# Performance work log

Measured on AMD Instinct MI355X. Metric: run time of the kernel, lower is better.

## Reference

```python
import jax, jax.numpy as jnp
import numpy as np

N = 512          # N_ROIs (nodes)
E = N * N        # number of edges
V = 6            # number of views (edge_attr dim)
DIMS = [(1, 36), (36, 24), (24, 5)]  # (in, out) per NNConv layer


def _nnconv(x, edge_attr, src, dst, We, be, root, bias, cin, cout):
    # edge MLP: Linear + ReLU -> per-edge weight matrix [E, cin, cout]
    w = jax.nn.relu(edge_attr @ We + be).reshape(-1, cin, cout)
    msg = jnp.einsum('ei,eio->eo', x[src], w)              # gather + per-edge matmul
    s = jax.ops.segment_sum(msg, dst, num_segments=N)      # scatter-sum
    cnt = jax.ops.segment_sum(jnp.ones((msg.shape[0], 1), x.dtype), dst, num_segments=N)
    agg = s / jnp.maximum(cnt, 1.0)                        # mean aggregation
    return agg + x @ root + bias                           # root weight + bias (PyG NNConv)


def setup_inputs() -> dict:
    key = jax.random.key(0)
    ks = jax.random.split(key, 16)
    x = jnp.ones((N, 1), jnp.float32)
    edge_attr = jax.random.uniform(ks[0], (E, V), jnp.float32)
    edge_index = jax.random.randint(ks[1], (2, E), 0, N, dtype=jnp.int32)
    inp = {'x': x, 'edge_attr': edge_attr, 'edge_index': edge_index}
    for l, (cin, cout) in enumerate(DIMS, start=1):
        k = jax.random.split(ks[1 + l], 4)
        inp[f'We{l}'] = jax.random.normal(k[0], (V, cin * cout), jnp.float32) / np.sqrt(V)
        inp[f'be{l}'] = jnp.zeros((cin * cout,), jnp.float32)
        inp[f'root{l}'] = jax.random.normal(k[1], (cin, cout), jnp.float32) / np.sqrt(cin)
        inp[f'b{l}'] = jnp.zeros((cout,), jnp.float32)
    return inp


def reference(x, edge_attr, edge_index,
              We1, be1, root1, b1,
              We2, be2, root2, b2,
              We3, be3, root3, b3):
    src, dst = edge_index[0], edge_index[1]
    h = jax.nn.relu(_nnconv(x, edge_attr, src, dst, We1, be1, root1, b1, *DIMS[0]))
    h = jax.nn.relu(_nnconv(h, edge_attr, src, dst, We2, be2, root2, b2, *DIMS[1]))
    h = jax.nn.relu(_nnconv(h, edge_attr, src, dst, We3, be3, root3, b3, *DIMS[2]))
    # pairwise CBT: sum_k |h_i,k - h_j,k|  ->  [N, N]
    cbt = jnp.sum(jnp.abs(h[:, None, :] - h[None, :, :]), axis=2)
    return cbt
```

## Files before the change

### kernel.cpp

```cpp
#include <hip/hip_runtime.h>
#include <hip/hip_bf16.h>

#define N_NODES 512
#define N_EDGES (512 * 512)
#define NBLK 256
#define EPB (N_EDGES / NBLK)

typedef __attribute__((ext_vector_type(2))) _Float16 half2v;

#if defined(__has_builtin)
#if __has_builtin(__builtin_amdgcn_fdot2)
#define FDOT2(a, b, c) __builtin_amdgcn_fdot2((a), (b), (c), false)
#endif
#endif
#ifndef FDOT2
static __device__ inline float fdot2_sw(half2v a, half2v b, float c) {
    return (float)a.x * (float)b.x + (float)a.y * (float)b.y + c;
}
#define FDOT2(a, b, c) fdot2_sw((a), (b), (c))
#endif

static __device__ inline unsigned pack_h2(float x, float y) {
    union { _Float16 h[2]; unsigned u; } c;
    c.h[0] = (_Float16)x;
    c.h[1] = (_Float16)y;
    return c.u;
}
static __device__ inline half2v bits_h2(int b) {
    union { int i; half2v h; } c;
    c.i = b;
    return c.h;
}

__global__ __launch_bounds__(256) void count_kernel(const int* __restrict__ dst,
                                                    int* __restrict__ bcnt) {
    __shared__ int h[N_NODES];
    int tid = threadIdx.x;
    int b = blockIdx.x;
    h[tid] = 0;
    h[tid + 256] = 0;
    __syncthreads();
#pragma unroll
    for (int k = 0; k < EPB / 256; k++)
        atomicAdd(&h[dst[b * EPB + k * 256 + tid]], 1);
    __syncthreads();
    bcnt[b * N_NODES + tid] = h[tid];
    bcnt[b * N_NODES + tid + 256] = h[tid + 256];
}

__global__ __launch_bounds__(512) void scan_kernel(const int* __restrict__ bcnt,
                                                   int* __restrict__ offs,
                                                   int* __restrict__ base) {
    __shared__ int buf[N_NODES];
    int t = threadIdx.x;
    int sum = 0;
    for (int b = 0; b < NBLK; b++) sum += bcnt[b * N_NODES + t];
    buf[t] = sum;
    __syncthreads();
    for (int d = 1; d < N_NODES; d <<= 1) {
        int add = (t >= d) ? buf[t - d] : 0;
        __syncthreads();
        buf[t] += add;
        __syncthreads();
    }
    offs[t + 1] = buf[t];
    if (t == 0) offs[0] = 0;
    int run = buf[t] - sum;
    for (int b = 0; b < NBLK; b++) {
        base[b * N_NODES + t] = run;
        run += bcnt[b * N_NODES + t];
    }
}

__global__ __launch_bounds__(256) void scatter_kernel(const int* __restrict__ src,
                                                      const int* __restrict__ dst,
                                                      const float* __restrict__ ea,
                                                      const int* __restrict__ base,
                                                      int4* __restrict__ ed4) {
    __shared__ int lcur[N_NODES];
    int tid = threadIdx.x;
    int b = blockIdx.x;
    lcur[tid] = base[b * N_NODES + tid];
    lcur[tid + 256] = base[b * N_NODES + tid + 256];
    __syncthreads();
#pragma unroll
    for (int k = 0; k < EPB / 256; k++) {
        int e = b * EPB + k * 256 + tid;
        const float* a = ea + (size_t)e * 6;
        float a0 = a[0], a1 = a[1], a2 = a[2], a3 = a[3], a4 = a[4], a5 = a[5];
        int p = atomicAdd(&lcur[dst[e]], 1);
        int4 r;
        r.x = (int)pack_h2(a0, a1);
        r.y = (int)pack_h2(a2, a3);
        r.z = (int)pack_h2(a4, a5);
        r.w = src[e];
        ed4[p] = r;
    }
}

template <int CIN, int COUT, int OG, int BLK, int G>
__global__ __launch_bounds__(BLK) void nnconv_edges(
    const float* __restrict__ hprev,
    const int4* __restrict__ ed4,
    const int* __restrict__ offs,
    const float* __restrict__ We,
    const float* __restrict__ be,
    float* __restrict__ agg)
{
    constexpr int J = CIN * COUT;
    constexpr int OPL = COUT / OG;
    constexpr int A = CIN * OPL;

    const int n = blockIdx.x / G;
    const int g = blockIdx.x % G;
    const int tid = threadIdx.x;
    const bool act = (tid < A);
    const int i = act ? tid / OPL : 0;
    const int og = act ? (tid % OPL) * OG : 0;

    half2v wrp[OG][3];
    float ber[OG], acc[OG];
#pragma unroll
    for (int k = 0; k < OG; k++) {
        acc[k] = 0.f;
        int j = i * COUT + og + k;
        if (act) {
            ber[k] = be[j];
#pragma unroll
            for (int t = 0; t < 3; t++)
                wrp[k][t] = bits_h2((int)pack_h2(We[(2 * t) * J + j], We[(2 * t + 1) * J + j]));
        } else {
            ber[k] = 0.f;
#pragma unroll
            for (int t = 0; t < 3; t++) wrp[k][t] = bits_h2(0);
        }
    }

    const int start = offs[n];
    const int end = offs[n + 1];
    const int len = end - start;
    const int per = (len + G - 1) / G;
    int p = start + g * per;
    int p1 = p + per;
    if (p1 > end) p1 = end;

    const float* hp_i = hprev + i;

    for (; p + 8 <= p1; p += 8) {
        const int4* eb = ed4 + p;
        int4 ed[8];
#pragma unroll
        for (int u = 0; u < 8; u++) ed[u] = eb[u];
        float xv[8];
#pragma unroll
        for (int u = 0; u < 8; u++) xv[u] = hp_i[ed[u].w * CIN];
#pragma unroll
        for (int u = 0; u < 8; u++) {
            half2v e01 = bits_h2(ed[u].x), e23 = bits_h2(ed[u].y), e45 = bits_h2(ed[u].z);
#pragma unroll
            for (int k = 0; k < OG; k++) {
                float z = FDOT2(e45, wrp[k][2],
                        FDOT2(e23, wrp[k][1],
                        FDOT2(e01, wrp[k][0], ber[k])));
                acc[k] = fmaf(xv[u], fmaxf(z, 0.f), acc[k]);
            }
        }
    }
    for (; p < p1; ++p) {
        int4 ed = ed4[p];
        float xv = hp_i[ed.w * CIN];
        half2v e01 = bits_h2(ed.x), e23 = bits_h2(ed.y), e45 = bits_h2(ed.z);
#pragma unroll
        for (int k = 0; k < OG; k++) {
            float z = FDOT2(e45, wrp[k][2],
                    FDOT2(e23, wrp[k][1],
                    FDOT2(e01, wrp[k][0], ber[k])));
            acc[k] = fmaf(xv, fmaxf(z, 0.f), acc[k]);
        }
    }

    if constexpr (CIN == 1) {
        if (act) atomicAdd(&agg[n * COUT + og], acc[0]);
    } else {
        __shared__ float lds_acc[J];
        if (act) {
#pragma unroll
            for (int k = 0; k < OG; k++) lds_acc[i * COUT + og + k] = acc[k];
        }
        __syncthreads();
        if (tid < COUT) {
            float sum = 0.f;
#pragma unroll
            for (int ii = 0; ii < CIN; ii++) sum += lds_acc[ii * COUT + tid];
            atomicAdd(&agg[n * COUT + tid], sum);
        }
    }
}

template <int CIN, int COUT>
__global__ __launch_bounds__(64) void nnconv_fin(const float* __restrict__ agg,
                                                 const int* __restrict__ offs,
                                                 const float* __restrict__ hprev,
                                                 const float* __restrict__ root,
                                                 const float* __restrict__ bias,
                                                 float* __restrict__ hout) {
    int n = blockIdx.x;
    int t = threadIdx.x;
    if (t >= COUT) return;
    int cnt = offs[n + 1] - offs[n];
    float inv = 1.f / fmaxf((float)cnt, 1.f);
    float v = agg[n * COUT + t] * inv;
#pragma unroll
    for (int i = 0; i < CIN; i++) v = fmaf(hprev[n * CIN + i], root[i * COUT + t], v);
    v += bias[t];
    hout[n * COUT + t] = fmaxf(v, 0.f);
}

__global__ __launch_bounds__(256) void cbt_kernel(const float* __restrict__ h3,
                                                  float* __restrict__ out) {
    __shared__ float lh[N_NODES * 5];
    int tid = threadIdx.x;
    for (int idx = tid; idx < N_NODES * 5; idx += 256) lh[idx] = h3[idx];
    __syncthreads();
    int i = blockIdx.x;
    float hi[5];
#pragma unroll
    for (int k = 0; k < 5; k++) hi[k] = lh[i * 5 + k];
    for (int j = tid; j < N_NODES; j += 256) {
        float sacc = 0.f;
#pragma unroll
        for (int k = 0; k < 5; k++) sacc += fabsf(hi[k] - lh[j * 5 + k]);
        out[i * N_NODES + j] = sacc;
    }
}

extern "C" void kernel_launch(void* const* d_in, const int* in_sizes, int n_in,
                              void* d_out, int out_size, void* d_ws, size_t ws_size,
                              hipStream_t stream) {
    const float* x = (const float*)d_in[0];
    const float* edge_attr = (const float*)d_in[1];
    const int* edge_index = (const int*)d_in[2];
    const float* We1 = (const float*)d_in[3];
    const float* be1 = (const float*)d_in[4];
    const float* root1 = (const float*)d_in[5];
    const float* b1 = (const float*)d_in[6];
    const float* We2 = (const float*)d_in[7];
    const float* be2 = (const float*)d_in[8];
    const float* root2 = (const float*)d_in[9];
    const float* b2 = (const float*)d_in[10];
    const float* We3 = (const float*)d_in[11];
    const float* be3 = (const float*)d_in[12];
    const float* root3 = (const float*)d_in[13];
    const float* b3 = (const float*)d_in[14];

    const int E = N_EDGES;
    const int* src = edge_index;
    const int* dst = edge_index + E;

    char* ws = (char*)d_ws;
    int* offs = (int*)(ws + 0);
    int* bcnt = (int*)(ws + 4096);
    int* base = (int*)(ws + 528384);
    int4* ed4 = (int4*)(ws + 1052672);
    float* agg1 = (float*)(ws + 5246976);
    float* agg2 = (float*)(ws + 5320704);
    float* agg3 = (float*)(ws + 5369856);
    float* h1 = (float*)(ws + 5380096);
    float* h2 = (float*)(ws + 5453824);
    float* h3 = (float*)(ws + 5502976);

    hipMemsetAsync(agg1, 0, 5380096 - 5246976, stream);

    count_kernel<<<NBLK, 256, 0, stream>>>(dst, bcnt);
    scan_kernel<<<1, 512, 0, stream>>>(bcnt, offs, base);
    scatter_kernel<<<NBLK, 256, 0, stream>>>(src, dst, edge_attr, base, ed4);

    nnconv_edges<1, 36, 1, 64, 16><<<N_NODES * 16, 64, 0, stream>>>(x, ed4, offs, We1, be1, agg1);
    nnconv_fin<1, 36><<<N_NODES, 64, 0, stream>>>(agg1, offs, x, root1, b1, h1);

    nnconv_edges<36, 24, 4, 256, 8><<<N_NODES * 8, 256, 0, stream>>>(h1, ed4, offs, We2, be2, agg2);
    nnconv_fin<36, 24><<<N_NODES, 64, 0, stream>>>(agg2, offs, h1, root2, b2, h2);

    nnconv_edges<24, 5, 1, 128, 8><<<N_NODES * 8, 128, 0, stream>>>(h2, ed4, offs, We3, be3, agg3);
    nnconv_fin<24, 5><<<N_NODES, 64, 0, stream>>>(agg3, offs, h2, root3, b3, h3);

    cbt_kernel<<<N_NODES, 256, 0, stream>>>(h3, (float*)d_out);
}
```

Measured before the change: 202.5 us.

## Compute NNConv edge MLP with bf16 MFMA over padded per-node edge tiles

```diff
diff --git a/kernel.cpp b/kernel.cpp
--- a/kernel.cpp
+++ b/kernel.cpp
@@ -1,35 +1,27 @@
 #include <hip/hip_runtime.h>
 #include <hip/hip_bf16.h>
+#include <hip/hip_fp16.h>
 
 #define N_NODES 512
 #define N_EDGES (512 * 512)
 #define NBLK 256
 #define EPB (N_EDGES / NBLK)
-
-typedef __attribute__((ext_vector_type(2))) _Float16 half2v;
-
-#if defined(__has_builtin)
-#if __has_builtin(__builtin_amdgcn_fdot2)
-#define FDOT2(a, b, c) __builtin_amdgcn_fdot2((a), (b), (c), false)
-#endif
-#endif
-#ifndef FDOT2
-static __device__ inline float fdot2_sw(half2v a, half2v b, float c) {
-    return (float)a.x * (float)b.x + (float)a.y * (float)b.y + c;
-}
-#define FDOT2(a, b, c) fdot2_sw((a), (b), (c))
-#endif
-
-static __device__ inline unsigned pack_h2(float x, float y) {
-    union { _Float16 h[2]; unsigned u; } c;
-    c.h[0] = (_Float16)x;
-    c.h[1] = (_Float16)y;
-    return c.u;
-}
-static __device__ inline half2v bits_h2(int b) {
-    union { int i; half2v h; } c;
-    c.i = b;
-    return c.h;
+#define PADLEN 768
+
+typedef __attribute__((ext_vector_type(8))) __bf16 bf16x8;
+typedef __attribute__((ext_vector_type(16))) float f32x16;
+
+static __device__ inline unsigned bf16rne(float f) {
+    union { float f; unsigned u; } c;
+    c.f = f;
+    unsigned u = c.u;
+    u += 0x7FFFu + ((u >> 16) & 1u);
+    return u >> 16;
+}
+static __device__ inline float bf2f(unsigned h) {
+    union { unsigned u; float f; } c;
+    c.u = h << 16;
+    return c.f;
 }
 
 __global__ __launch_bounds__(256) void count_kernel(const int* __restrict__ dst,
@@ -54,6 +46,7 @@
     __shared__ int buf[N_NODES];
     int t = threadIdx.x;
     int sum = 0;
+#pragma unroll 16
     for (int b = 0; b < NBLK; b++) sum += bcnt[b * N_NODES + t];
     buf[t] = sum;
     __syncthreads();
@@ -66,6 +59,7 @@
     offs[t + 1] = buf[t];
     if (t == 0) offs[0] = 0;
     int run = buf[t] - sum;
+#pragma unroll 16
     for (int b = 0; b < NBLK; b++) {
         base[b * N_NODES + t] = run;
         run += bcnt[b * N_NODES + t];
@@ -76,144 +70,171 @@
                                                       const int* __restrict__ dst,
                                                       const float* __restrict__ ea,
                                                       const int* __restrict__ base,
-                                                      int4* __restrict__ ed4) {
+                                                      const int* __restrict__ offs,
+                                                      int4* __restrict__ edp,
+                                                      int* __restrict__ srcp) {
     __shared__ int lcur[N_NODES];
+    __shared__ int loff[N_NODES];
     int tid = threadIdx.x;
     int b = blockIdx.x;
     lcur[tid] = base[b * N_NODES + tid];
     lcur[tid + 256] = base[b * N_NODES + tid + 256];
-    __syncthreads();
+    loff[tid] = offs[tid];
+    loff[tid + 256] = offs[tid + 256];
+    __syncthreads();
+    const unsigned ONE = 0x3F80u;
 #pragma unroll
     for (int k = 0; k < EPB / 256; k++) {
         int e = b * EPB + k * 256 + tid;
         const float* a = ea + (size_t)e * 6;
-        float a0 = a[0], a1 = a[1], a2 = a[2], a3 = a[3], a4 = a[4], a5 = a[5];
-        int p = atomicAdd(&lcur[dst[e]], 1);
-        int4 r;
-        r.x = (int)pack_h2(a0, a1);
-        r.y = (int)pack_h2(a2, a3);
-        r.z = (int)pack_h2(a4, a5);
-        r.w = src[e];
-        ed4[p] = r;
-    }
-}
-
-template <int CIN, int COUT, int OG, int BLK, int G>
-__global__ __launch_bounds__(BLK) void nnconv_edges(
+        unsigned e0 = bf16rne(a[0]), e1 = bf16rne(a[1]), e2 = bf16rne(a[2]);
+        unsigned e3 = bf16rne(a[3]), e4 = bf16rne(a[4]), e5 = bf16rne(a[5]);
+        int dv = dst[e], sv = src[e];
+        int p = atomicAdd(&lcur[dv], 1);
+        int rank = p - loff[dv];
+        size_t pi = (size_t)dv * PADLEN + rank;
+        int4 r0, r1;
+        r0.x = (int)((e1 << 16) | e0);
+        r0.y = (int)((e3 << 16) | e2);
+        r0.z = (int)((e5 << 16) | e4);
+        r0.w = (int)((e0 << 16) | ONE);
+        r1.x = (int)((e2 << 16) | e1);
+        r1.y = (int)((e4 << 16) | e3);
+        r1.z = (int)((ONE << 16) | e5);
+        r1.w = 0;
+        edp[pi * 2] = r0;
+        edp[pi * 2 + 1] = r1;
+        srcp[pi] = sv;
+    }
+}
+
+__global__ __launch_bounds__(256) void wprep_kernel(const float* __restrict__ We,
+                                                    const float* __restrict__ be,
+                                                    int Jr, int total,
+                                                    int4* __restrict__ wtg) {
+    int idx = blockIdx.x * 256 + threadIdx.x;
+    if (idx >= total) return;
+    int t = idx >> 6, lane = idx & 63, col = lane & 31, hi = lane >> 5;
+    int j = t * 32 + col;
+    unsigned h[8] = {0, 0, 0, 0, 0, 0, 0, 0};
+    if (j < Jr) {
+        unsigned wh[6];
+        float wl[6];
+        for (int v = 0; v < 6; v++) {
+            float wv = We[v * Jr + j];
+            wh[v] = bf16rne(wv);
+            wl[v] = wv - bf2f(wh[v]);
+        }
+        float bev = be[j];
+        unsigned bh = bf16rne(bev);
+        float bl = bev - bf2f(bh);
+        if (hi == 0) {
+            for (int v = 0; v < 6; v++) h[v] = wh[v];
+            h[6] = bh;
+            h[7] = bf16rne(wl[0]);
+        } else {
+            for (int v = 1; v < 6; v++) h[v - 1] = bf16rne(wl[v]);
+            h[5] = bf16rne(bl);
+            h[6] = 0;
+            h[7] = 0;
+        }
+    }
+    int4 r;
+    r.x = (int)((h[1] << 16) | h[0]);
+    r.y = (int)((h[3] << 16) | h[2]);
+    r.z = (int)((h[5] << 16) | h[4]);
+    r.w = (int)((h[7] << 16) | h[6]);
+    wtg[idx] = r;
+}
+
+template <int CIN, int COUT, int TILES, int SLOTS>
+__global__ __launch_bounds__(512, 4) void nnconv_mfma(
     const float* __restrict__ hprev,
-    const int4* __restrict__ ed4,
+    const int4* __restrict__ edp,
+    const int* __restrict__ srcp,
     const int* __restrict__ offs,
-    const float* __restrict__ We,
-    const float* __restrict__ be,
-    float* __restrict__ agg)
+    const int4* __restrict__ wtg,
+    const float* __restrict__ root,
+    const float* __restrict__ bias,
+    float* __restrict__ hout)
 {
-    constexpr int J = CIN * COUT;
-    constexpr int OPL = COUT / OG;
-    constexpr int A = CIN * OPL;
-
-    const int n = blockIdx.x / G;
-    const int g = blockIdx.x % G;
+    __shared__ __half xs[N_NODES * CIN];
+    __shared__ int4 wl[TILES * 64];
+    __shared__ float lagg[COUT];
+
     const int tid = threadIdx.x;
-    const bool act = (tid < A);
-    const int i = act ? tid / OPL : 0;
-    const int og = act ? (tid % OPL) * OG : 0;
-
-    half2v wrp[OG][3];
-    float ber[OG], acc[OG];
-#pragma unroll
-    for (int k = 0; k < OG; k++) {
-        acc[k] = 0.f;
-        int j = i * COUT + og + k;
-        if (act) {
-            ber[k] = be[j];
-#pragma unroll
-            for (int t = 0; t < 3; t++)
-                wrp[k][t] = bits_h2((int)pack_h2(We[(2 * t) * J + j], We[(2 * t + 1) * J + j]));
-        } else {
-            ber[k] = 0.f;
-#pragma unroll
-            for (int t = 0; t < 3; t++) wrp[k][t] = bits_h2(0);
+    const int n = blockIdx.x;
+
+    for (int k = tid; k < N_NODES * CIN; k += 512) xs[k] = __float2half(hprev[k]);
+    for (int k = tid; k < TILES * 64; k += 512) wl[k] = wtg[k];
+    if (tid < COUT) lagg[tid] = 0.f;
+    __syncthreads();
+
+    const int w = tid >> 6, lane = tid & 63;
+    const int col = lane & 31, hi = lane >> 5;
+    const char* xsp = (const char*)xs;
+    const char* wlp = (const char*)wl + (hi * 32 + col) * 16;
+
+    f32x16 zc;
+#pragma unroll
+    for (int q = 0; q < 16; q++) zc[q] = 0.f;
+
+    float ao[SLOTS];
+#pragma unroll
+    for (int s = 0; s < SLOTS; s++) ao[s] = 0.f;
+
+    const int nb = n * PADLEN + w * 96;
+
+    for (int c = 0; c < 3; c++) {
+        const int cb = nb + c * 32;
+        bf16x8 af = *(const bf16x8*)((const char*)edp + (size_t)(cb + col) * 32 + hi * 16);
+        int xb[16];
+#pragma unroll
+        for (int qq = 0; qq < 4; qq++) {
+            int4 sv = *(const int4*)(srcp + cb + qq * 8 + hi * 4);
+            xb[qq * 4 + 0] = sv.x * (CIN * 2);
+            xb[qq * 4 + 1] = sv.y * (CIN * 2);
+            xb[qq * 4 + 2] = sv.z * (CIN * 2);
+            xb[qq * 4 + 3] = sv.w * (CIN * 2);
         }
-    }
-
-    const int start = offs[n];
-    const int end = offs[n + 1];
-    const int len = end - start;
-    const int per = (len + G - 1) / G;
-    int p = start + g * per;
-    int p1 = p + per;
-    if (p1 > end) p1 = end;
-
-    const float* hp_i = hprev + i;
-
-    for (; p + 8 <= p1; p += 8) {
-        const int4* eb = ed4 + p;
-        int4 ed[8];
-#pragma unroll
-        for (int u = 0; u < 8; u++) ed[u] = eb[u];
-        float xv[8];
-#pragma unroll
-        for (int u = 0; u < 8; u++) xv[u] = hp_i[ed[u].w * CIN];
-#pragma unroll
-        for (int u = 0; u < 8; u++) {
-            half2v e01 = bits_h2(ed[u].x), e23 = bits_h2(ed[u].y), e45 = bits_h2(ed[u].z);
-#pragma unroll
-            for (int k = 0; k < OG; k++) {
-                float z = FDOT2(e45, wrp[k][2],
-                        FDOT2(e23, wrp[k][1],
-                        FDOT2(e01, wrp[k][0], ber[k])));
-                acc[k] = fmaf(xv[u], fmaxf(z, 0.f), acc[k]);
+        const char* wq = wlp;
+        int jb = col;
+#pragma unroll 1
+        for (int tt = 0; tt < TILES / SLOTS; tt++) {
+#pragma unroll
+            for (int s = 0; s < SLOTS; s++) {
+                bf16x8 bf = *(const bf16x8*)(wq + s * 1024);
+                f32x16 ct = __builtin_amdgcn_mfma_f32_32x32x16_bf16(af, bf, zc, 0, 0, 0);
+                int j = jb + s * 32;
+                int i = j / COUT;
+                if (i > CIN - 1) i = CIN - 1;
+                int i2 = i * 2;
+#pragma unroll
+                for (int r = 0; r < 16; r++) {
+                    float xv = __half2float(*(const __half*)(xsp + xb[r] + i2));
+                    ao[s] = fmaf(fmaxf(ct[r], 0.f), xv, ao[s]);
+                }
             }
+            wq += SLOTS * 1024;
+            jb += SLOTS * 32;
         }
     }
-    for (; p < p1; ++p) {
-        int4 ed = ed4[p];
-        float xv = hp_i[ed.w * CIN];
-        half2v e01 = bits_h2(ed.x), e23 = bits_h2(ed.y), e45 = bits_h2(ed.z);
-#pragma unroll
-        for (int k = 0; k < OG; k++) {
-            float z = FDOT2(e45, wrp[k][2],
-                    FDOT2(e23, wrp[k][1],
-                    FDOT2(e01, wrp[k][0], ber[k])));
-            acc[k] = fmaf(xv, fmaxf(z, 0.f), acc[k]);
-        }
-    }
-
-    if constexpr (CIN == 1) {
-        if (act) atomicAdd(&agg[n * COUT + og], acc[0]);
-    } else {
-        __shared__ float lds_acc[J];
-        if (act) {
-#pragma unroll
-            for (int k = 0; k < OG; k++) lds_acc[i * COUT + og + k] = acc[k];
-        }
-        __syncthreads();
-        if (tid < COUT) {
-            float sum = 0.f;
-#pragma unroll
-            for (int ii = 0; ii < CIN; ii++) sum += lds_acc[ii * COUT + tid];
-            atomicAdd(&agg[n * COUT + tid], sum);
-        }
-    }
-}
-
-template <int CIN, int COUT>
-__global__ __launch_bounds__(64) void nnconv_fin(const float* __restrict__ agg,
-                                                 const int* __restrict__ offs,
-                                                 const float* __restrict__ hprev,
-                                                 const float* __restrict__ root,
-                                                 const float* __restrict__ bias,
-                                                 float* __restrict__ hout) {
-    int n = blockIdx.x;
-    int t = threadIdx.x;
-    if (t >= COUT) return;
-    int cnt = offs[n + 1] - offs[n];
-    float inv = 1.f / fmaxf((float)cnt, 1.f);
-    float v = agg[n * COUT + t] * inv;
-#pragma unroll
-    for (int i = 0; i < CIN; i++) v = fmaf(hprev[n * CIN + i], root[i * COUT + t], v);
-    v += bias[t];
-    hout[n * COUT + t] = fmaxf(v, 0.f);
+
+#pragma unroll
+    for (int s = 0; s < SLOTS; s++) {
+        int o = (s * 32 + col) % COUT;
+        atomicAdd(&lagg[o], ao[s]);
+    }
+    __syncthreads();
+
+    if (tid < COUT) {
+        int cnt = offs[n + 1] - offs[n];
+        float v = lagg[tid] / fmaxf((float)cnt, 1.f);
+#pragma unroll
+        for (int i = 0; i < CIN; i++)
+            v = fmaf(hprev[n * CIN + i], root[i * COUT + tid], v);
+        hout[n * COUT + tid] = fmaxf(v + bias[tid], 0.f);
+    }
 }
 
 __global__ __launch_bounds__(256) void cbt_kernel(const float* __restrict__ h3,
@@ -261,28 +282,28 @@
     int* offs = (int*)(ws + 0);
     int* bcnt = (int*)(ws + 4096);
     int* base = (int*)(ws + 528384);
-    int4* ed4 = (int4*)(ws + 1052672);
-    float* agg1 = (float*)(ws + 5246976);
-    float* agg2 = (float*)(ws + 5320704);
-    float* agg3 = (float*)(ws + 5369856);
-    float* h1 = (float*)(ws + 5380096);
-    float* h2 = (float*)(ws + 5453824);
-    float* h3 = (float*)(ws + 5502976);
-
-    hipMemsetAsync(agg1, 0, 5380096 - 5246976, stream);
+    int4* edp = (int4*)(ws + 1052672);
+    int* srcp = (int*)(ws + 13635584);
+    int4* wtg1 = (int4*)(ws + 15208448);
+    int4* wtg2 = (int4*)(ws + 15210496);
+    int4* wtg3 = (int4*)(ws + 15238144);
+    float* h1 = (float*)(ws + 15242240);
+    float* h2 = (float*)(ws + 15315968);
+    float* h3 = (float*)(ws + 15365120);
+
+    hipMemsetAsync(edp, 0, (size_t)N_NODES * PADLEN * 32 + (size_t)N_NODES * PADLEN * 4, stream);
 
     count_kernel<<<NBLK, 256, 0, stream>>>(dst, bcnt);
     scan_kernel<<<1, 512, 0, stream>>>(bcnt, offs, base);
-    scatter_kernel<<<NBLK, 256, 0, stream>>>(src, dst, edge_attr, base, ed4);
-
-    nnconv_edges<1, 36, 1, 64, 16><<<N_NODES * 16, 64, 0, stream>>>(x, ed4, offs, We1, be1, agg1);
-    nnconv_fin<1, 36><<<N_NODES, 64, 0, stream>>>(agg1, offs, x, root1, b1, h1);
-
-    nnconv_edges<36, 24, 4, 256, 8><<<N_NODES * 8, 256, 0, stream>>>(h1, ed4, offs, We2, be2, agg2);
-    nnconv_fin<36, 24><<<N_NODES, 64, 0, stream>>>(agg2, offs, h1, root2, b2, h2);
-
-    nnconv_edges<24, 5, 1, 128, 8><<<N_NODES * 8, 128, 0, stream>>>(h2, ed4, offs, We3, be3, agg3);
-    nnconv_fin<24, 5><<<N_NODES, 64, 0, stream>>>(agg3, offs, h2, root3, b3, h3);
+    scatter_kernel<<<NBLK, 256, 0, stream>>>(src, dst, edge_attr, base, offs, edp, srcp);
+
+    wprep_kernel<<<1, 256, 0, stream>>>(We1, be1, 36, 2 * 64, wtg1);
+    wprep_kernel<<<7, 256, 0, stream>>>(We2, be2, 864, 27 * 64, wtg2);
+    wprep_kernel<<<1, 256, 0, stream>>>(We3, be3, 120, 4 * 64, wtg3);
+
+    nnconv_mfma<1, 36, 2, 2><<<N_NODES, 512, 0, stream>>>(x, edp, srcp, offs, wtg1, root1, b1, h1);
+    nnconv_mfma<36, 24, 27, 3><<<N_NODES, 512, 0, stream>>>(h1, edp, srcp, offs, wtg2, root2, b2, h2);
+    nnconv_mfma<24, 5, 4, 4><<<N_NODES, 512, 0, stream>>>(h2, edp, srcp, offs, wtg3, root3, b3, h3);
 
     cbt_kernel<<<N_NODES, 256, 0, stream>>>(h3, (float*)d_out);
 }
```

After: 220.2 us. +8.7%, slower.
